# Kernel tuning notes

Hardware: AMD Instinct MI355X
Metric: run time of the kernel (lower is better)

## Reference

```python
import jax, jax.numpy as jnp
import numpy as np

N = 100_000      # nodes
E = 1_600_000    # nonzeros of the rescaled Laplacian (avg degree 16)
F_IN = 128
F_OUT = 128
K = 4


def setup_inputs() -> dict:
    key = jax.random.key(0)
    ks = jax.random.split(key, 6)
    x = jax.random.normal(ks[0], (N, F_IN), dtype=jnp.float32)
    filter_coeff = jax.random.normal(ks[1], (K, N), dtype=jnp.float32)
    # glorot-ish scale for [K, F_in, F_out]
    stdv = float(np.sqrt(6.0 / (F_IN + F_OUT)))
    weight = jax.random.uniform(ks[2], (K, F_IN, F_OUT), dtype=jnp.float32,
                                minval=-stdv, maxval=stdv)
    bias = jnp.zeros((F_OUT,), dtype=jnp.float32)
    src = jax.random.randint(ks[3], (E,), 0, N, dtype=jnp.int32)
    dst = jax.random.randint(ks[4], (E,), 0, N, dtype=jnp.int32)
    # edge values of L_hat = 2L/lambda_max - I (precomputed sparse matrix)
    edge_w = jax.random.normal(ks[5], (E,), dtype=jnp.float32) * 0.1
    return {"x": x, "filter_coeff": filter_coeff, "weight": weight,
            "bias": bias, "edge_w": edge_w, "src": src, "dst": dst}


def reference(x, filter_coeff, weight, bias, edge_w, src, dst):
    n = x.shape[0]

    def spmm(h):  # edge-weighted gather-scale-segment_sum == dgl.update_all
        return jax.ops.segment_sum(h[src] * edge_w[:, None], dst,
                                   num_segments=n)

    # Chebyshev recurrence: T0 = x, T1 = L_hat x, T_k = 2 L_hat T_{k-1} - T_{k-2}
    Tx0 = x
    out = (filter_coeff[0][:, None] * Tx0) @ weight[0]
    Tx1 = spmm(x)
    out = out + (filter_coeff[1][:, None] * Tx1) @ weight[1]
    for k in range(2, weight.shape[0]):
        Tx2 = 2.0 * spmm(Tx1) - Tx0
        out = out + (filter_coeff[k][:, None] * Tx2) @ weight[k]
        Tx0, Tx1 = Tx1, Tx2
    return out + bias
```

## Files before the change

### kernel.cpp

```cpp
#include <hip/hip_runtime.h>
#include <hip/hip_bf16.h>
#include <cstdio>

#define F 128
#define BSHIFT 9
#define BROWS 512
#define C2 4096

typedef __attribute__((ext_vector_type(4))) float f32x4;
typedef __attribute__((ext_vector_type(4))) unsigned short u16x4;
typedef __attribute__((ext_vector_type(8))) short s16x8;

__device__ inline unsigned short f2bf(float x) {
  unsigned int u = __float_as_uint(x);
  u += 0x7fffu + ((u >> 16) & 1u);
  return (unsigned short)(u >> 16);
}
__device__ inline float bf2f(unsigned int h) {
  return __uint_as_float(h << 16);
}

__device__ inline void async_load16(const void* g, void* l) {
  __builtin_amdgcn_global_load_lds(
      (const __attribute__((address_space(1))) void*)g,
      (__attribute__((address_space(3))) void*)l, 16, 0, 0);
}

__global__ void bucket_hist_kernel(const int* __restrict__ dst, int* __restrict__ bhist,
                                   int E, int B) {
  __shared__ int h[256];
  int t = threadIdx.x;
  h[t] = 0;
  __syncthreads();
  for (int e = blockIdx.x * blockDim.x + t; e < E; e += gridDim.x * blockDim.x)
    atomicAdd(&h[dst[e] >> BSHIFT], 1);
  __syncthreads();
  if (t < B && h[t]) atomicAdd(&bhist[t], h[t]);
}

__global__ void bucket_scan_kernel(const int* __restrict__ bhist, int* __restrict__ bbase,
                                   int* __restrict__ bcursor, int* __restrict__ rp,
                                   int E, int B, int N) {
  __shared__ int sm[256];
  int t = threadIdx.x;
  int v = (t < B) ? bhist[t] : 0;
  sm[t] = v;
  __syncthreads();
  int x = v;
  for (int off = 1; off < 256; off <<= 1) {
    int add = (t >= off) ? sm[t - off] : 0;
    __syncthreads();
    x += add;
    sm[t] = x;
    __syncthreads();
  }
  int excl = x - v;
  if (t < B) { bbase[t] = excl; bcursor[t] = excl; }
  if (t == 0) { bbase[B] = E; rp[N] = E; }
}

__global__ __launch_bounds__(256) void bucket_scatter_kernel(
    const int* __restrict__ src, const int* __restrict__ dst, const float* __restrict__ ew,
    int* __restrict__ bcursor, unsigned int* __restrict__ stg_p, float* __restrict__ stg_w,
    int E, int B) {
  __shared__ int hist[256], gbase[256], cur[256], sm[256], scn[256];
  __shared__ unsigned int sp[C2];
  __shared__ float swt[C2];
  __shared__ int sdest[C2];
  int t = threadIdx.x;
  int e0 = blockIdx.x * C2;
  int cnt = min(C2, E - e0);
  hist[t] = 0;
  __syncthreads();
#pragma unroll
  for (int i = 0; i < C2 / 256; ++i) {
    int e = e0 + t + i * 256;
    if (e < E) atomicAdd(&hist[dst[e] >> BSHIFT], 1);
  }
  __syncthreads();
  int v = hist[t];
  gbase[t] = (t < B && v) ? atomicAdd(&bcursor[t], v) : 0;
  sm[t] = v;
  __syncthreads();
  int x = v;
  for (int off = 1; off < 256; off <<= 1) {
    int add = (t >= off) ? sm[t - off] : 0;
    __syncthreads();
    x += add;
    sm[t] = x;
    __syncthreads();
  }
  scn[t] = x - v;
  cur[t] = 0;
  __syncthreads();
#pragma unroll
  for (int i = 0; i < C2 / 256; ++i) {
    int e = e0 + t + i * 256;
    if (e < E) {
      int d = dst[e];
      int b = d >> BSHIFT;
      int r = atomicAdd(&cur[b], 1);
      int slot = scn[b] + r;
      sp[slot] = (unsigned int)src[e] | ((unsigned int)(d & (BROWS - 1)) << 17);
      swt[slot] = ew[e];
      sdest[slot] = gbase[b] + r;
    }
  }
  __syncthreads();
#pragma unroll
  for (int i = 0; i < C2 / 256; ++i) {
    int s = t + i * 256;
    if (s < cnt) {
      int dpos = sdest[s];
      stg_p[dpos] = sp[s];
      stg_w[dpos] = swt[s];
    }
  }
}

__global__ __launch_bounds__(256) void csr_build_kernel(
    const unsigned int* __restrict__ stg_p, const float* __restrict__ stg_w,
    const int* __restrict__ bbase, int* __restrict__ rp, int2* __restrict__ csr,
    int N, int B) {
  __shared__ int rhist[BROWS], rloc[BROWS], curp[BROWS];
  __shared__ int sm[256];
  int b = blockIdx.x, t = threadIdx.x;
  int row0 = b << BSHIFT;
  int base = bbase[b];
  int cnt = bbase[b + 1] - base;
  rhist[t] = 0;
  rhist[t + 256] = 0;
  __syncthreads();
  for (int s = base + t; s < base + cnt; s += 256)
    atomicAdd(&rhist[stg_p[s] >> 17], 1);
  __syncthreads();
  int a0 = rhist[2 * t], a1 = rhist[2 * t + 1];
  int pv = a0 + a1;
  sm[t] = pv;
  __syncthreads();
  int x = pv;
  for (int off = 1; off < 256; off <<= 1) {
    int add = (t >= off) ? sm[t - off] : 0;
    __syncthreads();
    x += add;
    sm[t] = x;
    __syncthreads();
  }
  int pexcl = x - pv;
  int r0 = 2 * t, r1 = 2 * t + 1;
  rloc[r0] = pexcl;
  rloc[r1] = pexcl + a0;
  if (row0 + r0 < N) rp[row0 + r0] = base + rloc[r0];
  if (row0 + r1 < N) rp[row0 + r1] = base + rloc[r1];
  curp[r0] = base + rloc[r0];
  curp[r1] = base + rloc[r1];
  __syncthreads();
  for (int s = base + t; s < base + cnt; s += 256) {
    unsigned int p = stg_p[s];
    int dl = p >> 17;
    int pos = atomicAdd(&curp[dl], 1);
    int2 entry;
    entry.x = (int)(p & 0x1ffffu);
    entry.y = __float_as_int(stg_w[s]);
    csr[pos] = entry;
  }
}

__global__ void convx_kernel(const float* __restrict__ x, unsigned short* __restrict__ xbf,
                             int total4) {
  int i = blockIdx.x * 256 + threadIdx.x;
  if (i >= total4) return;
  f32x4 v = ((const f32x4*)x)[i];
  u16x4 o;
  o.x = f2bf(v.x); o.y = f2bf(v.y); o.z = f2bf(v.z); o.w = f2bf(v.w);
  ((u16x4*)xbf)[i] = o;
}

__global__ __launch_bounds__(256) void spmm_kernel(
    const unsigned short* __restrict__ Tin, const unsigned short* __restrict__ Tsub,
    unsigned short* __restrict__ Tout, const int* __restrict__ rp,
    const int2* __restrict__ csr, int n, float scale) {
  int row = blockIdx.x * 16 + (threadIdx.x >> 4);
  if (row >= n) return;
  int sl = threadIdx.x & 15;
  int j0 = rp[row], end = rp[row + 1];
  const uint4* Tin4 = (const uint4*)Tin;
  float acc[8];
#pragma unroll
  for (int c = 0; c < 8; ++c) acc[c] = 0.f;

  for (int j = j0; j < end; j += 8) {
    int2 e[8];
#pragma unroll
    for (int u = 0; u < 8; ++u)
      if (j + u < end) e[u] = csr[j + u];
    uint4 v[8];
#pragma unroll
    for (int u = 0; u < 8; ++u)
      if (j + u < end) v[u] = Tin4[(size_t)e[u].x * 16 + sl];
#pragma unroll
    for (int u = 0; u < 8; ++u) {
      if (j + u < end) {
        float w = __int_as_float(e[u].y);
        acc[0] = fmaf(w, bf2f(v[u].x & 0xffffu), acc[0]);
        acc[1] = fmaf(w, bf2f(v[u].x >> 16), acc[1]);
        acc[2] = fmaf(w, bf2f(v[u].y & 0xffffu), acc[2]);
        acc[3] = fmaf(w, bf2f(v[u].y >> 16), acc[3]);
        acc[4] = fmaf(w, bf2f(v[u].z & 0xffffu), acc[4]);
        acc[5] = fmaf(w, bf2f(v[u].z >> 16), acc[5]);
        acc[6] = fmaf(w, bf2f(v[u].w & 0xffffu), acc[6]);
        acc[7] = fmaf(w, bf2f(v[u].w >> 16), acc[7]);
      }
    }
  }

  float r[8];
#pragma unroll
  for (int c = 0; c < 8; ++c) r[c] = scale * acc[c];
  if (Tsub) {
    uint4 p = ((const uint4*)Tsub)[(size_t)row * 16 + sl];
    r[0] -= bf2f(p.x & 0xffffu); r[1] -= bf2f(p.x >> 16);
    r[2] -= bf2f(p.y & 0xffffu); r[3] -= bf2f(p.y >> 16);
    r[4] -= bf2f(p.z & 0xffffu); r[5] -= bf2f(p.z >> 16);
    r[6] -= bf2f(p.w & 0xffffu); r[7] -= bf2f(p.w >> 16);
  }
  uint4 o;
  o.x = (unsigned)f2bf(r[0]) | ((unsigned)f2bf(r[1]) << 16);
  o.y = (unsigned)f2bf(r[2]) | ((unsigned)f2bf(r[3]) << 16);
  o.z = (unsigned)f2bf(r[4]) | ((unsigned)f2bf(r[5]) << 16);
  o.w = (unsigned)f2bf(r[6]) | ((unsigned)f2bf(r[7]) << 16);
  ((uint4*)Tout)[(size_t)row * 16 + sl] = o;
}

__global__ void convw_kernel(const float* __restrict__ W, unsigned short* __restrict__ Wf,
                             int total) {
  int idx = blockIdx.x * 256 + threadIdx.x;
  if (idx >= total) return;
  int j = idx & 7;
  int lane = (idx >> 3) & 63;
  int nt = (idx >> 9) & 7;
  int kk = (idx >> 12) & 3;
  int ks = idx >> 14;
  int kl = kk * 32 + (lane >> 4) * 8 + j;
  int col = nt * 16 + (lane & 15);
  Wf[idx] = f2bf(W[(size_t)ks * F * F + (size_t)kl * F + col]);
}

struct GemmArgs {
  const unsigned short* A[8];
  const float* fc;
  const unsigned short* Wt;
  const float* bias;
  float* out;
  int n;
  int kslices;
};

__global__ __launch_bounds__(512) void gemm_kernel(GemmArgs args) {
  __shared__ __align__(16) unsigned short SA[2][16384];
  __shared__ __align__(16) unsigned short SB[2][16384];
  const int t = threadIdx.x;
  const int lane = t & 63;
  const int wid = t >> 6;
  const int wrow = wid >> 1;
  const int wcol = wid & 1;
  const int n = args.n;
  const int KS = args.kslices;
  const int bm = blockIdx.x * 128;
  const int arow = lane & 15;
  const int kg = lane >> 4;

  auto stage = [&](int ks, int b) {
    const unsigned short* As = args.A[ks];
#pragma unroll
    for (int i = 0; i < 4; ++i) {
      int fi = wid + i * 8;
      int rg = fi >> 2, kk = fi & 3;
      int r = bm + rg * 16 + arow;
      if (r >= n) r = n - 1;
      async_load16((const void*)(As + (size_t)r * F + kk * 32 + kg * 8),
                   (void*)(SA[b] + fi * 512));
    }
#pragma unroll
    for (int i = 0; i < 4; ++i) {
      int fi = wid + i * 8;
      async_load16((const void*)(args.Wt + (size_t)ks * 16384 + fi * 512 + lane * 8),
                   (void*)(SB[b] + fi * 512));
    }
  };

  f32x4 Cf[2][4];
#pragma unroll
  for (int mt = 0; mt < 2; ++mt)
#pragma unroll
    for (int nt = 0; nt < 4; ++nt) Cf[mt][nt] = (f32x4){0.f, 0.f, 0.f, 0.f};

  int row_c[2];
#pragma unroll
  for (int mt = 0; mt < 2; ++mt) {
    int r = bm + wrow * 32 + mt * 16 + arow;
    row_c[mt] = r < n ? r : n - 1;
  }

  stage(0, 0);

  for (int ks = 0; ks < KS; ++ks) {
    const int b = ks & 1;
    if (ks + 1 < KS) {
      stage(ks + 1, b ^ 1);
      asm volatile("s_waitcnt vmcnt(8)" ::: "memory");
    } else {
      asm volatile("s_waitcnt vmcnt(0)" ::: "memory");
    }
    __builtin_amdgcn_sched_barrier(0);
    __builtin_amdgcn_s_barrier();
    __builtin_amdgcn_sched_barrier(0);

    float fv[2];
#pragma unroll
    for (int mt = 0; mt < 2; ++mt) fv[mt] = args.fc[(size_t)ks * n + row_c[mt]];

    f32x4 acc[2][4];
#pragma unroll
    for (int mt = 0; mt < 2; ++mt)
#pragma unroll
      for (int nt = 0; nt < 4; ++nt) acc[mt][nt] = (f32x4){0.f, 0.f, 0.f, 0.f};

#pragma unroll
    for (int kk = 0; kk < 4; ++kk) {
      s16x8 af[2], bfr[4];
#pragma unroll
      for (int mt = 0; mt < 2; ++mt) {
        int rg = wrow * 2 + mt;
        af[mt] = *(const s16x8*)&SA[b][(rg * 4 + kk) * 512 + lane * 8];
      }
#pragma unroll
      for (int nt = 0; nt < 4; ++nt)
        bfr[nt] = *(const s16x8*)&SB[b][(kk * 8 + wcol * 4 + nt) * 512 + lane * 8];
#pragma unroll
      for (int mt = 0; mt < 2; ++mt)
#pragma unroll
        for (int nt = 0; nt < 4; ++nt)
          acc[mt][nt] = __builtin_amdgcn_mfma_f32_16x16x32_bf16(bfr[nt], af[mt],
                                                                acc[mt][nt], 0, 0, 0);
    }

#pragma unroll
    for (int mt = 0; mt < 2; ++mt)
#pragma unroll
      for (int nt = 0; nt < 4; ++nt) Cf[mt][nt] += fv[mt] * acc[mt][nt];

    __builtin_amdgcn_sched_barrier(0);
    __builtin_amdgcn_s_barrier();
    __builtin_amdgcn_sched_barrier(0);
  }

#pragma unroll
  for (int mt = 0; mt < 2; ++mt) {
    int row = bm + wrow * 32 + mt * 16 + arow;
    if (row >= n) continue;
#pragma unroll
    for (int nt = 0; nt < 4; ++nt) {
      int col = (wcol * 4 + nt) * 16 + kg * 4;
      f32x4 bv = *(const f32x4*)(args.bias + col);
      *(f32x4*)(args.out + (size_t)row * F + col) = Cf[mt][nt] + bv;
    }
  }
}

extern "C" void kernel_launch(void* const* d_in, const int* in_sizes, int n_in,
                              void* d_out, int out_size, void* d_ws, size_t ws_size,
                              hipStream_t stream) {
  const float* x    = (const float*)d_in[0];
  const float* fc   = (const float*)d_in[1];
  const float* W    = (const float*)d_in[2];
  const float* bias = (const float*)d_in[3];
  const float* ew   = (const float*)d_in[4];
  const int*   src  = (const int*)d_in[5];
  const int*   dst  = (const int*)d_in[6];

  const int N = in_sizes[0] / F;
  const int K = in_sizes[2] / (F * F);
  const int E = in_sizes[4];
  const int B = (N + BROWS - 1) >> BSHIFT;

  size_t off = 0;
  char* base = (char*)d_ws;
  auto alloc = [&](size_t bytes) -> void* {
    void* p = base + off;
    off += (bytes + 511) & ~(size_t)511;
    return p;
  };
  int* rp              = (int*)alloc(((size_t)N + 1) * 4);
  int* bhist           = (int*)alloc(1024);
  int* bbase           = (int*)alloc(1040);
  int* bcursor         = (int*)alloc(1024);
  int2* csr            = (int2*)alloc((size_t)E * 8);
  unsigned short* Wt   = (unsigned short*)alloc((size_t)K * F * F * 2);
  unsigned short* xbf  = (unsigned short*)alloc((size_t)N * F * 2);
  unsigned short* T[8];
  T[0] = xbf;
  for (int k = 1; k < K && k < 8; ++k) T[k] = (unsigned short*)alloc((size_t)N * F * 2);
  unsigned int* stg_p;
  float* stg_w;
  if (K >= 3 && (size_t)N * F * 2 >= (size_t)E * 8) {
    stg_p = (unsigned int*)T[2];
    stg_w = (float*)(T[2] + (size_t)E * 2);
  } else {
    stg_p = (unsigned int*)alloc((size_t)E * 4);
    stg_w = (float*)alloc((size_t)E * 4);
  }
  if (off > ws_size) {
    fprintf(stderr, "kernel_launch: ws too small: need %zu have %zu\n", off, ws_size);
    return;
  }

  hipMemsetAsync(bhist, 0, 1024, stream);
  hipLaunchKernelGGL(bucket_hist_kernel, dim3(208), dim3(256), 0, stream, dst, bhist, E, B);
  hipLaunchKernelGGL(bucket_scan_kernel, dim3(1), dim3(256), 0, stream, bhist, bbase, bcursor,
                     rp, E, B, N);
  int sblocks = (E + C2 - 1) / C2;
  hipLaunchKernelGGL(bucket_scatter_kernel, dim3(sblocks), dim3(256), 0, stream, src, dst, ew,
                     bcursor, stg_p, stg_w, E, B);
  hipLaunchKernelGGL(csr_build_kernel, dim3(B), dim3(256), 0, stream, stg_p, stg_w, bbase,
                     rp, csr, N, B);

  int total4 = N * F / 4;
  hipLaunchKernelGGL(convx_kernel, dim3((total4 + 255) / 256), dim3(256), 0, stream,
                     x, xbf, total4);

  int sb = (N + 15) / 16;
  if (K > 1)
    hipLaunchKernelGGL(spmm_kernel, dim3(sb), dim3(256), 0, stream, xbf,
                       (const unsigned short*)nullptr, T[1], rp, csr, N, 1.0f);
  for (int k = 2; k < K; ++k) {
    const unsigned short* prev = T[k - 2];
    hipLaunchKernelGGL(spmm_kernel, dim3(sb), dim3(256), 0, stream, T[k - 1], prev, T[k],
                       rp, csr, N, 2.0f);
  }

  int total = K * F * F;
  hipLaunchKernelGGL(convw_kernel, dim3((total + 255) / 256), dim3(256), 0, stream, W, Wt,
                     total);

  GemmArgs ga;
  for (int k = 0; k < 8; ++k) ga.A[k] = (k < K) ? T[k] : xbf;
  ga.fc = fc; ga.Wt = Wt; ga.bias = bias;
  ga.out = (float*)d_out;
  ga.n = N; ga.kslices = K;
  hipLaunchKernelGGL(gemm_kernel, dim3((N + 127) / 128), dim3(512), 0, stream, ga);
}
```

Baseline: 320.3 us.

## Slice features into 16-column panels so SpMM gathers hit L2-resident slices

Stores the bf16 Chebyshev terms in a column-sliced layout: eight panels of 16 features, each panel contiguous over all rows. The SpMM grid now gives each block one panel and 128 rows, with two threads per row, so the random gathers for a panel touch only a 3.2 MB working set that can stay in cache. CSR and Tsub reads and the output writes use nontemporal hints. The GEMM loader is changed to read the new layout. In exchange, the CSR is re-read once per panel (eight times), the inner unroll drops to 4, and each gather is only 32 bytes.

After: 889.0 us. 178% more time.

```diff
diff --git a/kernel.cpp b/kernel.cpp
--- a/kernel.cpp
+++ b/kernel.cpp
@@ -10,6 +10,8 @@
 typedef __attribute__((ext_vector_type(4))) float f32x4;
 typedef __attribute__((ext_vector_type(4))) unsigned short u16x4;
 typedef __attribute__((ext_vector_type(8))) short s16x8;
+typedef __attribute__((ext_vector_type(4))) unsigned int u32x4;
+typedef __attribute__((ext_vector_type(2))) int i32x2;
 
 __device__ inline unsigned short f2bf(float x) {
   unsigned int u = __float_as_uint(x);
@@ -166,40 +168,50 @@
   }
 }
 
-__global__ void convx_kernel(const float* __restrict__ x, unsigned short* __restrict__ xbf,
-                             int total4) {
-  int i = blockIdx.x * 256 + threadIdx.x;
-  if (i >= total4) return;
-  f32x4 v = ((const f32x4*)x)[i];
-  u16x4 o;
-  o.x = f2bf(v.x); o.y = f2bf(v.y); o.z = f2bf(v.z); o.w = f2bf(v.w);
-  ((u16x4*)xbf)[i] = o;
+__global__ void convx_kernel(const float* __restrict__ x, unsigned short* __restrict__ xs,
+                             int n) {
+  int idx = blockIdx.x * 256 + threadIdx.x;
+  if (idx >= n * 16) return;
+  int h = idx & 1, s = (idx >> 1) & 7, row = idx >> 4;
+  const float* srcp = x + (size_t)row * 128 + s * 16 + h * 8;
+  f32x4 a = *(const f32x4*)srcp;
+  f32x4 b = *(const f32x4*)(srcp + 4);
+  u16x4 o0, o1;
+  o0.x = f2bf(a.x); o0.y = f2bf(a.y); o0.z = f2bf(a.z); o0.w = f2bf(a.w);
+  o1.x = f2bf(b.x); o1.y = f2bf(b.y); o1.z = f2bf(b.z); o1.w = f2bf(b.w);
+  unsigned short* d = xs + ((size_t)s * n + row) * 16 + h * 8;
+  *(u16x4*)d = o0;
+  *(u16x4*)(d + 4) = o1;
 }
 
 __global__ __launch_bounds__(256) void spmm_kernel(
     const unsigned short* __restrict__ Tin, const unsigned short* __restrict__ Tsub,
     unsigned short* __restrict__ Tout, const int* __restrict__ rp,
     const int2* __restrict__ csr, int n, float scale) {
-  int row = blockIdx.x * 16 + (threadIdx.x >> 4);
+  const int s = blockIdx.x & 7;
+  const int rb = blockIdx.x >> 3;
+  const int pair = threadIdx.x >> 1;
+  const int h = threadIdx.x & 1;
+  const int row = rb * 128 + pair;
   if (row >= n) return;
-  int sl = threadIdx.x & 15;
-  int j0 = rp[row], end = rp[row + 1];
-  const uint4* Tin4 = (const uint4*)Tin;
+  const size_t sbase = (size_t)s * n * 16;
+  const unsigned short* Tins = Tin + sbase;
+  const int end = rp[row + 1];
   float acc[8];
 #pragma unroll
   for (int c = 0; c < 8; ++c) acc[c] = 0.f;
 
-  for (int j = j0; j < end; j += 8) {
-    int2 e[8];
-#pragma unroll
-    for (int u = 0; u < 8; ++u)
-      if (j + u < end) e[u] = csr[j + u];
-    uint4 v[8];
-#pragma unroll
-    for (int u = 0; u < 8; ++u)
-      if (j + u < end) v[u] = Tin4[(size_t)e[u].x * 16 + sl];
-#pragma unroll
-    for (int u = 0; u < 8; ++u) {
+  for (int j = rp[row]; j < end; j += 4) {
+    i32x2 e[4];
+    u32x4 v[4];
+#pragma unroll
+    for (int u = 0; u < 4; ++u)
+      if (j + u < end) e[u] = __builtin_nontemporal_load((const i32x2*)(csr + j + u));
+#pragma unroll
+    for (int u = 0; u < 4; ++u)
+      if (j + u < end) v[u] = *(const u32x4*)(Tins + (size_t)e[u].x * 16 + h * 8);
+#pragma unroll
+    for (int u = 0; u < 4; ++u) {
       if (j + u < end) {
         float w = __int_as_float(e[u].y);
         acc[0] = fmaf(w, bf2f(v[u].x & 0xffffu), acc[0]);
@@ -218,18 +230,19 @@
 #pragma unroll
   for (int c = 0; c < 8; ++c) r[c] = scale * acc[c];
   if (Tsub) {
-    uint4 p = ((const uint4*)Tsub)[(size_t)row * 16 + sl];
+    u32x4 p = __builtin_nontemporal_load(
+        (const u32x4*)(Tsub + sbase + (size_t)row * 16 + h * 8));
     r[0] -= bf2f(p.x & 0xffffu); r[1] -= bf2f(p.x >> 16);
     r[2] -= bf2f(p.y & 0xffffu); r[3] -= bf2f(p.y >> 16);
     r[4] -= bf2f(p.z & 0xffffu); r[5] -= bf2f(p.z >> 16);
     r[6] -= bf2f(p.w & 0xffffu); r[7] -= bf2f(p.w >> 16);
   }
-  uint4 o;
+  u32x4 o;
   o.x = (unsigned)f2bf(r[0]) | ((unsigned)f2bf(r[1]) << 16);
   o.y = (unsigned)f2bf(r[2]) | ((unsigned)f2bf(r[3]) << 16);
   o.z = (unsigned)f2bf(r[4]) | ((unsigned)f2bf(r[5]) << 16);
   o.w = (unsigned)f2bf(r[6]) | ((unsigned)f2bf(r[7]) << 16);
-  ((uint4*)Tout)[(size_t)row * 16 + sl] = o;
+  __builtin_nontemporal_store(o, (u32x4*)(Tout + sbase + (size_t)row * 16 + h * 8));
 }
 
 __global__ void convw_kernel(const float* __restrict__ W, unsigned short* __restrict__ Wf,
@@ -278,8 +291,9 @@
       int rg = fi >> 2, kk = fi & 3;
       int r = bm + rg * 16 + arow;
       if (r >= n) r = n - 1;
-      async_load16((const void*)(As + (size_t)r * F + kk * 32 + kg * 8),
-                   (void*)(SA[b] + fi * 512));
+      int col = kk * 32 + kg * 8;
+      const void* g = (const void*)(As + ((size_t)(col >> 4) * n + r) * 16 + (col & 15));
+      async_load16(g, (void*)(SA[b] + fi * 512));
     }
 #pragma unroll
     for (int i = 0; i < 4; ++i) {
@@ -425,11 +439,10 @@
   hipLaunchKernelGGL(csr_build_kernel, dim3(B), dim3(256), 0, stream, stg_p, stg_w, bbase,
                      rp, csr, N, B);
 
-  int total4 = N * F / 4;
-  hipLaunchKernelGGL(convx_kernel, dim3((total4 + 255) / 256), dim3(256), 0, stream,
-                     x, xbf, total4);
-
-  int sb = (N + 15) / 16;
+  hipLaunchKernelGGL(convx_kernel, dim3((N * 16 + 255) / 256), dim3(256), 0, stream,
+                     x, xbf, N);
+
+  int sb = ((N + 127) / 128) * 8;
   if (K > 1)
     hipLaunchKernelGGL(spmm_kernel, dim3(sb), dim3(256), 0, stream, xbf,
                        (const unsigned short*)nullptr, T[1], rp, csr, N, 1.0f);
```
